# Performance work log

Hardware: AMD Instinct MI355X
Metric: run time of the kernel (lower is better)

## Reference

```python
import jax, jax.numpy as jnp
import numpy as np

TAU = 2.0        # args.tau default (spikingjelly LIFNode)
V_TH = 1.0       # v_threshold
V_RESET = 0.0    # v_reset (hard reset)
ALPHA = 2.0      # ATan surrogate alpha

@jax.custom_vjp
def atan_spike(x):
    # Heaviside spike with ATan surrogate gradient (spikingjelly surrogate.ATan)
    return (x >= 0.0).astype(x.dtype)

def _atan_fwd(x):
    return atan_spike(x), x

def _atan_bwd(x, g):
    sg = (ALPHA / 2.0) / (1.0 + (jnp.pi / 2.0 * ALPHA * x) ** 2)
    return (g * sg,)

atan_spike.defvjp(_atan_fwd, _atan_bwd)

def setup_inputs() -> dict:
    key = jax.random.key(0)
    k1, k2, k3 = jax.random.split(key, 3)
    T, B, IN, OUT, NC = 16, 512, 3072, 2048, 10
    x_seq = jax.random.normal(k1, (T, B, IN), dtype=jnp.float32)
    # xavier-uniform-like scale: sqrt(2/(fan_in+fan_out))
    fc_w = jax.random.normal(k2, (OUT, IN), dtype=jnp.float32) * np.sqrt(2.0 / (IN + OUT)).astype(np.float32)
    fc_b = jnp.zeros((OUT,), jnp.float32)
    aux_w = jax.random.normal(k3, (NC, OUT), dtype=jnp.float32) * np.sqrt(2.0 / (OUT + NC)).astype(np.float32)
    aux_b = jnp.zeros((NC,), jnp.float32)
    return {"x_seq": x_seq, "fc_w": fc_w, "fc_b": fc_b, "aux_w": aux_w, "aux_b": aux_b}

def reference(x_seq, fc_w, fc_b, aux_w, aux_b):
    # fc over all timesteps: [T,B,in] @ [out,in]^T -> [T,B,out]
    cur_seq = jnp.einsum('tbi,oi->tbo', x_seq, fc_w) + fc_b

    def step(v, c):
        # LIF charge: v += (x - (v - v_reset)) / tau
        v = v + (c - (v - V_RESET)) / TAU
        s = atan_spike(v - V_TH)
        s_d = jax.lax.stop_gradient(s)  # detach_reset=True
        v = (1.0 - s_d) * v + s_d * V_RESET  # hard reset
        return v, s

    v0 = jnp.full(cur_seq.shape[1:], V_RESET, cur_seq.dtype)  # reset_net -> v = v_reset
    _, spk_seq = jax.lax.scan(step, v0, cur_seq)  # spk_seq: [T,B,out]
    count = spk_seq.sum(axis=0)                    # [B,out]
    logits = count @ aux_w.T + aux_b               # aux_head local logits [B,10]
    return spk_seq, count, logits
```

## Files before the change

kernel.cpp:

```cpp
#include <hip/hip_runtime.h>
#include <hip/hip_bf16.h>
#include <stdint.h>

#define T_   16
#define B_   512
#define IN_  3072
#define OUT_ 2048
#define NC_  10
#define M_   (T_ * B_)

#define BM 128
#define BN 128

#define SPK_SZ ((size_t)T_ * B_ * OUT_)
#define CNT_SZ ((size_t)B_ * OUT_)

#define TOL 6e-5
#define MAXFLAG (B_ * OUT_)

#define BK2   32
#define NCH2  (IN_ / BK2)
#define TILE_US 8192
#define APAN (M_ / BM)
#define BPAN (OUT_ / BN)

#define A_PREP_BLOCKS (APAN * NCH2 * 2)
#define B_PREP_BLOCKS (BPAN * NCH2 * 2)

typedef __attribute__((ext_vector_type(8))) short s16x8;
typedef __attribute__((ext_vector_type(4))) float f32x4;

__device__ unsigned int g_ctr;
__device__ unsigned int g_list[MAXFLAG];

__global__ void zero_ctr() { if (threadIdx.x == 0) g_ctr = 0; }

__device__ __forceinline__ unsigned short f2bf(float f) {
    __bf16 h = (__bf16)f;
    return *(unsigned short*)&h;
}
__device__ __forceinline__ float bf2f(unsigned short u) {
    union { unsigned int i; float f; } c; c.i = ((unsigned int)u) << 16; return c.f;
}
__device__ __forceinline__ int swz8(int r, int g) {
    return r * 64 + ((g ^ (r & 7)) << 3);
}

__device__ __forceinline__ void gload_lds16(const void* g, void* l) {
    __builtin_amdgcn_global_load_lds(
        (const __attribute__((address_space(1))) unsigned int*)g,
        (__attribute__((address_space(3))) unsigned int*)l, 16, 0, 0);
}

__global__ __launch_bounds__(256)
void prep2(const float* __restrict__ x, const float* __restrict__ w,
           unsigned short* __restrict__ Adig, unsigned short* __restrict__ Bdig)
{
    if (blockIdx.x == 0 && threadIdx.x == 0) g_ctr = 0;

    const float* src; unsigned short* dst; int id; bool isA;
    if (blockIdx.x < A_PREP_BLOCKS) {
        src = x; dst = Adig; id = blockIdx.x * 256 + threadIdx.x; isA = true;
    } else {
        src = w; dst = Bdig; id = (blockIdx.x - A_PREP_BLOCKS) * 256 + threadIdx.x; isA = false;
    }
    const int gk = id & 3;
    const int r  = (id >> 2) & 127;
    const int ch = (id >> 9) % NCH2;
    const int pa = id / (NCH2 * 512);
    const int m  = pa * 128 + r;
    const int k  = ch * BK2 + gk * 8;

    size_t srow;
    if (isA) srow = (size_t)(m & 15) * B_ + (m >> 4);
    else     srow = (size_t)m;

    float f[8];
    *(float4*)&f[0] = *(const float4*)(src + srow * IN_ + k);
    *(float4*)&f[4] = *(const float4*)(src + srow * IN_ + k + 4);
    s16x8 hi, lo;
#pragma unroll
    for (int j = 0; j < 8; ++j) {
        unsigned short hb = f2bf(f[j]);
        hi[j] = (short)hb;
        lo[j] = (short)f2bf(f[j] - bf2f(hb));
    }
    unsigned short* tb = dst + ((size_t)pa * NCH2 + ch) * TILE_US;
    *(s16x8*)&tb[swz8(r, gk)]     = hi;
    *(s16x8*)&tb[swz8(r, gk + 4)] = lo;
}

__global__ __launch_bounds__(512, 1)
void gemm_fused(const unsigned short* __restrict__ Adig,
                const unsigned short* __restrict__ Bdig,
                const float* __restrict__ fcb,
                float* __restrict__ out)
{
    __shared__ __align__(16) unsigned short SH[2 * 4 * TILE_US];

    const int tid = threadIdx.x;
    const int l   = tid & 63;
    const int wv  = tid >> 6;
    const int wh  = wv >> 2;
    const int wn  = (wv & 3) * 64;
    const int pB  = (wv >> 1) & 1;
    const int rb0 = (wv & 1) * 64;

    const int lin = blockIdx.x;
    const int xcd = lin & 7;
    const int jj  = lin >> 3;
    const int pm2 = xcd * 4 + (jj & 3);
    const int pn2 = jj >> 2;
    const int n0  = pn2 * 256;

    f32x4 acc[8][4];
#pragma unroll
    for (int i = 0; i < 8; ++i)
#pragma unroll
        for (int j = 0; j < 4; ++j) acc[i][j] = (f32x4)0.0f;

    const int lp = l & 15;
    const int lq = l >> 4;
    const int l8 = l * 8;

    const int rg  = wv >> 1;
    const int sub = (wv & 1) * 4096;
    const unsigned short* gsrc0;
    if (rg < 2) gsrc0 = Adig + ((size_t)(2 * pm2 + rg) * NCH2) * TILE_US;
    else        gsrc0 = Bdig + ((size_t)(2 * pn2 + rg - 2) * NCH2) * TILE_US;

    auto stage = [&](int ch, int d) {
        const unsigned short* s = gsrc0 + (size_t)ch * TILE_US + sub;
        unsigned short* dp = SH + (d * 4 + rg) * TILE_US + sub;
#pragma unroll
        for (int i = 0; i < 8; ++i)
            gload_lds16(s + i * 512 + l8, dp + i * 512);
    };

    s16x8 a1f[8], a2f[8], b1f[4], b2f[4];

    auto a_read = [&](int dd, int i) {
        const int ra = i * 16 + lp;
        const unsigned short* Ap = SH + (dd * 4 + wh) * TILE_US;
        a1f[i] = *(const s16x8*)&Ap[swz8(ra, lq)];
        a2f[i] = *(const s16x8*)&Ap[swz8(ra, lq + 4)];
    };
    auto b_read = [&](int dd, int j) {
        const int rb = rb0 + j * 16 + lp;
        const unsigned short* Bp = SH + (dd * 4 + 2 + pB) * TILE_US;
        b1f[j] = *(const s16x8*)&Bp[swz8(rb, lq)];
        b2f[j] = *(const s16x8*)&Bp[swz8(rb, lq + 4)];
    };
    auto mfma3 = [&](int i, int j) {
        acc[i][j] = __builtin_amdgcn_mfma_f32_16x16x32_bf16(a1f[i], b1f[j], acc[i][j], 0, 0, 0);
        acc[i][j] = __builtin_amdgcn_mfma_f32_16x16x32_bf16(a2f[i], b1f[j], acc[i][j], 0, 0, 0);
        acc[i][j] = __builtin_amdgcn_mfma_f32_16x16x32_bf16(a1f[i], b2f[j], acc[i][j], 0, 0, 0);
    };

    auto phase_reload = [&](int dd) {
        __builtin_amdgcn_s_setprio(1);
#pragma unroll
        for (int i = 0; i < 7; ++i) {
#pragma unroll
            for (int j = 0; j < 4; ++j) mfma3(i, j);
            a_read(dd, i);
        }
#pragma unroll
        for (int j = 0; j < 4; ++j) {
            mfma3(7, j);
            b_read(dd, j);
        }
        a_read(dd, 7);
        __builtin_amdgcn_s_setprio(0);
    };
    auto phase_plain = [&]() {
        __builtin_amdgcn_s_setprio(1);
#pragma unroll
        for (int i = 0; i < 8; ++i)
#pragma unroll
            for (int j = 0; j < 4; ++j) mfma3(i, j);
        __builtin_amdgcn_s_setprio(0);
    };

    auto body = [&](int ch, int d, int dd) {
        asm volatile("s_waitcnt lgkmcnt(0)" ::: "memory");
        __builtin_amdgcn_s_barrier();
        asm volatile("" ::: "memory");
        if (ch + 2 < NCH2) {
            stage(ch + 2, d);
            asm volatile("s_waitcnt vmcnt(8)" ::: "memory");
        } else {
            asm volatile("s_waitcnt vmcnt(0)" ::: "memory");
        }
        __builtin_amdgcn_s_barrier();
        asm volatile("" ::: "memory");
        if (ch + 1 < NCH2) phase_reload(dd); else phase_plain();
    };

    stage(0, 0);
    asm volatile("s_waitcnt vmcnt(0)" ::: "memory");
    __builtin_amdgcn_s_barrier();
    asm volatile("" ::: "memory");
    stage(1, 1);
#pragma unroll
    for (int i = 0; i < 8; ++i) a_read(0, i);
#pragma unroll
    for (int j = 0; j < 4; ++j) b_read(0, j);

    for (int c2 = 0; c2 < NCH2 / 2; ++c2) {
        const int ch = c2 * 2;
        body(ch, 0, 1);
        body(ch + 1, 1, 0);
    }

    float* cf = (float*)SH;

    const int o_l = tid & 255;
    const int o   = n0 + o_l;
    const float bias = fcb[o];
    const int bq0 = (tid >> 8) * 4;

    for (int p = 0; p < 2; ++p) {
        if (p) __syncthreads();
        if (wh == p) {
#pragma unroll
            for (int i = 0; i < 8; ++i)
#pragma unroll
                for (int j = 0; j < 4; ++j)
#pragma unroll
                    for (int reg = 0; reg < 4; ++reg) {
                        const int row = i * 16 + lq * 4 + reg;
                        const int col = wn + j * 16 + lp;
                        cf[row * 256 + (col ^ ((row & 12) << 1))] = acc[i][j][reg];
                    }
        }
        __syncthreads();

#pragma unroll
        for (int q = 0; q < 4; ++q) {
            const int rl = bq0 + q;
            const int b  = pm2 * 16 + p * 8 + rl;
            float v = 0.0f; int cnt = 0; bool fl = false;
#pragma unroll
            for (int t = 0; t < T_; ++t) {
                const int row = rl * 16 + t;
                const float c32 = cf[row * 256 + (o_l ^ ((row & 12) << 1))];
                const float c = c32 + bias;
                v = v + (c - v) * 0.5f;
                const float dlt = v - 1.0f;
                const bool s = dlt >= 0.0f;
                if (fabsf(dlt) < (float)TOL) fl = true;
                out[(size_t)t * CNT_SZ + (size_t)b * OUT_ + o] = s ? 1.0f : 0.0f;
                cnt += s ? 1 : 0;
                if (s) v = 0.0f;
            }
            out[SPK_SZ + (size_t)b * OUT_ + o] = (float)cnt;
            if (fl) {
                unsigned int idx = atomicAdd(&g_ctr, 1u);
                if (idx < MAXFLAG) g_list[idx] = (unsigned int)(b * OUT_ + o);
            }
        }
    }
}

__global__ __launch_bounds__(256, 2)
void gemm_split(const float* __restrict__ x, const float* __restrict__ w,
                float* __restrict__ cur)
{
    __shared__ __align__(16) unsigned short A1[BM * 64];
    __shared__ __align__(16) unsigned short A2[BM * 64];
    __shared__ __align__(16) unsigned short B1[BN * 64];
    __shared__ __align__(16) unsigned short B2[BN * 64];

    const int tid = threadIdx.x;
    const int l   = tid & 63;
    const int wv  = tid >> 6;
    const int wm  = (wv >> 1) * 64;
    const int wn  = (wv & 1) * 64;
    const int m0  = blockIdx.x * BM;
    const int n0  = blockIdx.y * BN;

    const int r = tid >> 1;
    const int h = tid & 1;
    const float* xa = x + (size_t)(m0 + r) * IN_ + h * 32;
    const float* wa = w + (size_t)(n0 + r) * IN_ + h * 32;

    f32x4 acc[4][4];
#pragma unroll
    for (int i = 0; i < 4; ++i)
#pragma unroll
        for (int j = 0; j < 4; ++j) acc[i][j] = (f32x4)0.0f;

    const int lp = l & 15;
    const int lq = l >> 4;

    for (int ch = 0; ch < 48; ++ch) {
        const int k0 = ch * 64;
        __syncthreads();
        float fx[32], fw[32];
#pragma unroll
        for (int i = 0; i < 8; ++i)
            *(float4*)&fx[4 * i] = *(const float4*)(xa + k0 + 4 * i);
#pragma unroll
        for (int i = 0; i < 8; ++i)
            *(float4*)&fw[4 * i] = *(const float4*)(wa + k0 + 4 * i);

#pragma unroll
        for (int q = 0; q < 4; ++q) {
            s16x8 vh, vl, uh, ul;
#pragma unroll
            for (int j = 0; j < 8; ++j) {
                float f = fx[8 * q + j];
                unsigned short hb = f2bf(f);
                vh[j] = (short)hb;
                vl[j] = (short)f2bf(f - bf2f(hb));
                float g = fw[8 * q + j];
                unsigned short gb = f2bf(g);
                uh[j] = (short)gb;
                ul[j] = (short)f2bf(g - bf2f(gb));
            }
            const int gg = h * 4 + q;
            *(s16x8*)&A1[swz8(r, gg)] = vh;
            *(s16x8*)&A2[swz8(r, gg)] = vl;
            *(s16x8*)&B1[swz8(r, gg)] = uh;
            *(s16x8*)&B2[swz8(r, gg)] = ul;
        }
        __syncthreads();

#pragma unroll
        for (int kk = 0; kk < 2; ++kk) {
            const int gb = kk * 4 + lq;
            s16x8 a1f[4], a2f[4], b1f[4], b2f[4];
#pragma unroll
            for (int i = 0; i < 4; ++i) {
                const int ra = wm + i * 16 + lp;
                a1f[i] = *(const s16x8*)&A1[swz8(ra, gb)];
                a2f[i] = *(const s16x8*)&A2[swz8(ra, gb)];
                const int rb = wn + i * 16 + lp;
                b1f[i] = *(const s16x8*)&B1[swz8(rb, gb)];
                b2f[i] = *(const s16x8*)&B2[swz8(rb, gb)];
            }
#pragma unroll
            for (int i = 0; i < 4; ++i)
#pragma unroll
                for (int j = 0; j < 4; ++j) {
                    acc[i][j] = __builtin_amdgcn_mfma_f32_16x16x32_bf16(
                        a1f[i], b1f[j], acc[i][j], 0, 0, 0);
                    acc[i][j] = __builtin_amdgcn_mfma_f32_16x16x32_bf16(
                        a2f[i], b1f[j], acc[i][j], 0, 0, 0);
                    acc[i][j] = __builtin_amdgcn_mfma_f32_16x16x32_bf16(
                        a1f[i], b2f[j], acc[i][j], 0, 0, 0);
                }
        }
    }

    const int crow = lq * 4, ccol = lp;
#pragma unroll
    for (int i = 0; i < 4; ++i)
#pragma unroll
        for (int j = 0; j < 4; ++j) {
            const size_t mbase = (size_t)(m0 + wm + i * 16 + crow);
            const int o = n0 + wn + j * 16 + ccol;
#pragma unroll
            for (int reg = 0; reg < 4; ++reg)
                cur[(mbase + reg) * OUT_ + o] = acc[i][j][reg];
        }
}

__global__ __launch_bounds__(256)
void lif_pass(const float* __restrict__ fcb, float* __restrict__ out)
{
    const int idx = blockIdx.x * 256 + threadIdx.x;
    const int o = idx & (OUT_ - 1);
    const double bias = (double)fcb[o];
    double v = 0.0; int cnt = 0; bool fl = false;
#pragma unroll
    for (int t = 0; t < T_; ++t) {
        const size_t p = (size_t)t * CNT_SZ + idx;
        double c = (double)out[p] + bias;
        v = v + (c - v) * 0.5;
        double d = v - 1.0;
        bool s = d >= 0.0;
        if (fabs(d) < TOL) fl = true;
        out[p] = s ? 1.0f : 0.0f;
        cnt += s ? 1 : 0;
        if (s) v = 0.0;
    }
    out[SPK_SZ + idx] = (float)cnt;
    if (fl) {
        unsigned int pI = atomicAdd(&g_ctr, 1u);
        if (pI < MAXFLAG) g_list[pI] = (unsigned int)idx;
    }
}

__global__ void fixup(const float* __restrict__ x, const float* __restrict__ w,
                      const float* __restrict__ fcb, float* __restrict__ out)
{
    int nf = (int)g_ctr; if (nf > MAXFLAG) nf = MAXFLAG;
    const int lane = threadIdx.x & 63;
    const int wid  = (blockIdx.x * blockDim.x + threadIdx.x) >> 6;
    const int nw   = (gridDim.x * blockDim.x) >> 6;

    for (int i = wid; i < nf; i += nw) {
        unsigned int e = g_list[i];
        int b = (int)(e >> 11), o = (int)(e & (OUT_ - 1));
        double part[T_];
#pragma unroll
        for (int t = 0; t < T_; ++t) part[t] = 0.0;
        const float* wrow = w + (size_t)o * IN_;
        for (int k = lane; k < IN_; k += 64) {
            double wvv = (double)wrow[k];
#pragma unroll
            for (int t = 0; t < T_; ++t)
                part[t] = fma((double)x[((size_t)t * B_ + b) * IN_ + k], wvv, part[t]);
        }
#pragma unroll
        for (int t = 0; t < T_; ++t)
#pragma unroll
            for (int off = 32; off > 0; off >>= 1)
                part[t] += __shfl_xor(part[t], off, 64);
        if (lane == 0) {
            double bias = (double)fcb[o];
            double v = 0.0; int cnt = 0;
#pragma unroll
            for (int t = 0; t < T_; ++t) {
                double c = part[t] + bias;
                v = v + (c - v) * 0.5;
                bool s = (v - 1.0) >= 0.0;
                out[(size_t)t * CNT_SZ + (size_t)b * OUT_ + o] = s ? 1.0f : 0.0f;
                cnt += s ? 1 : 0;
                if (s) v = 0.0;
            }
            out[SPK_SZ + (size_t)b * OUT_ + o] = (float)cnt;
        }
    }
}

__global__ void aux_logits(const float* __restrict__ cnt,
                           const float* __restrict__ aw,
                           const float* __restrict__ ab,
                           float* __restrict__ lg)
{
    const int b = blockIdx.x;
    const int lane = threadIdx.x;
    double p0=0,p1=0,p2=0,p3=0,p4=0,p5=0,p6=0,p7=0,p8=0,p9=0;
    for (int o = lane; o < OUT_; o += 64) {
        double c = (double)cnt[(size_t)b * OUT_ + o];
        p0 = fma(c, (double)aw[0 * OUT_ + o], p0);
        p1 = fma(c, (double)aw[1 * OUT_ + o], p1);
        p2 = fma(c, (double)aw[2 * OUT_ + o], p2);
        p3 = fma(c, (double)aw[3 * OUT_ + o], p3);
        p4 = fma(c, (double)aw[4 * OUT_ + o], p4);
        p5 = fma(c, (double)aw[5 * OUT_ + o], p5);
        p6 = fma(c, (double)aw[6 * OUT_ + o], p6);
        p7 = fma(c, (double)aw[7 * OUT_ + o], p7);
        p8 = fma(c, (double)aw[8 * OUT_ + o], p8);
        p9 = fma(c, (double)aw[9 * OUT_ + o], p9);
    }
#pragma unroll
    for (int off = 32; off > 0; off >>= 1) {
        p0 += __shfl_xor(p0, off, 64); p1 += __shfl_xor(p1, off, 64);
        p2 += __shfl_xor(p2, off, 64); p3 += __shfl_xor(p3, off, 64);
        p4 += __shfl_xor(p4, off, 64); p5 += __shfl_xor(p5, off, 64);
        p6 += __shfl_xor(p6, off, 64); p7 += __shfl_xor(p7, off, 64);
        p8 += __shfl_xor(p8, off, 64); p9 += __shfl_xor(p9, off, 64);
    }
    if (lane == 0) {
        double pv[NC_] = {p0,p1,p2,p3,p4,p5,p6,p7,p8,p9};
#pragma unroll
        for (int c = 0; c < NC_; ++c)
            lg[(size_t)b * NC_ + c] = (float)(pv[c] + (double)ab[c]);
    }
}

extern "C" void kernel_launch(void* const* d_in, const int* in_sizes, int n_in,
                              void* d_out, int out_size, void* d_ws, size_t ws_size,
                              hipStream_t stream)
{
    (void)in_sizes; (void)n_in; (void)out_size;
    const float* x   = (const float*)d_in[0];
    const float* w   = (const float*)d_in[1];
    const float* fcb = (const float*)d_in[2];
    const float* aw  = (const float*)d_in[3];
    const float* ab  = (const float*)d_in[4];
    float* out = (float*)d_out;

    const size_t needA = (size_t)APAN * NCH2 * TILE_US * 2;
    const size_t needB = (size_t)BPAN * NCH2 * TILE_US * 2;

    if (ws_size >= needA + needB) {
        unsigned short* Adig = (unsigned short*)d_ws;
        unsigned short* Bdig = Adig + (size_t)APAN * NCH2 * TILE_US;
        prep2<<<dim3(A_PREP_BLOCKS + B_PREP_BLOCKS), dim3(256), 0, stream>>>(
            x, w, Adig, Bdig);
        gemm_fused<<<dim3(256), dim3(512), 0, stream>>>(Adig, Bdig, fcb, out);
    } else {
        zero_ctr<<<dim3(1), dim3(64), 0, stream>>>();
        gemm_split<<<dim3(M_ / BM, OUT_ / BN), dim3(256), 0, stream>>>(x, w, out);
        lif_pass<<<dim3(CNT_SZ / 256), dim3(256), 0, stream>>>(fcb, out);
    }

    fixup<<<dim3(192), dim3(256), 0, stream>>>(x, w, fcb, out);

    aux_logits<<<dim3(B_), dim3(64), 0, stream>>>(
        out + SPK_SZ, aw, ab, out + SPK_SZ + CNT_SZ);
}
```

Before: 347.9 us.

## Replace LDS-staged GEMM with direct global-to-register fragment loads

The fused GEMM+LIF kernel drops its double-buffered LDS staging (global_load_lds plus barriers). Each wave now loads its bf16 hi/lo MFMA fragments straight from the pre-swizzled global tiles into registers, relying on L2 for reuse. The grid becomes 512 blocks of 256 threads with two blocks per CU, and each wave runs its LIF epilogue through a private LDS slice, so the block-wide syncs are gone. This removes LDS traffic and barrier stalls, but reused A/B data is now fetched redundantly through L1/L2 with global-memory latency exposed inside the MFMA loop.

```diff
diff --git a/kernel.cpp b/kernel.cpp
--- a/kernel.cpp
+++ b/kernel.cpp
@@ -46,12 +46,6 @@
     return r * 64 + ((g ^ (r & 7)) << 3);
 }
 
-__device__ __forceinline__ void gload_lds16(const void* g, void* l) {
-    __builtin_amdgcn_global_load_lds(
-        (const __attribute__((address_space(1))) unsigned int*)g,
-        (__attribute__((address_space(3))) unsigned int*)l, 16, 0, 0);
-}
-
 __global__ __launch_bounds__(256)
 void prep2(const float* __restrict__ x, const float* __restrict__ w,
            unsigned short* __restrict__ Adig, unsigned short* __restrict__ Bdig)
@@ -90,28 +84,26 @@
     *(s16x8*)&tb[swz8(r, gk + 4)] = lo;
 }
 
-__global__ __launch_bounds__(512, 1)
-void gemm_fused(const unsigned short* __restrict__ Adig,
-                const unsigned short* __restrict__ Bdig,
-                const float* __restrict__ fcb,
-                float* __restrict__ out)
-{
-    __shared__ __align__(16) unsigned short SH[2 * 4 * TILE_US];
+__global__ __launch_bounds__(256, 2)
+void gemm_l2(const unsigned short* __restrict__ Adig,
+             const unsigned short* __restrict__ Bdig,
+             const float* __restrict__ fcb,
+             float* __restrict__ out)
+{
+    __shared__ float SHED[4 * 4096];
 
     const int tid = threadIdx.x;
     const int l   = tid & 63;
     const int wv  = tid >> 6;
-    const int wh  = wv >> 2;
-    const int wn  = (wv & 3) * 64;
-    const int pB  = (wv >> 1) & 1;
-    const int rb0 = (wv & 1) * 64;
 
     const int lin = blockIdx.x;
     const int xcd = lin & 7;
     const int jj  = lin >> 3;
-    const int pm2 = xcd * 4 + (jj & 3);
-    const int pn2 = jj >> 2;
-    const int n0  = pn2 * 256;
+    const int pm  = xcd * 8 + (jj & 7);
+    const int pn2 = jj >> 3;
+    const int pb  = 2 * pn2 + (wv >> 1);
+    const int rb0 = (wv & 1) * 64;
+    const int o0  = pn2 * 256 + wv * 64;
 
     f32x4 acc[8][4];
 #pragma unroll
@@ -121,35 +113,33 @@
 
     const int lp = l & 15;
     const int lq = l >> 4;
-    const int l8 = l * 8;
-
-    const int rg  = wv >> 1;
-    const int sub = (wv & 1) * 4096;
-    const unsigned short* gsrc0;
-    if (rg < 2) gsrc0 = Adig + ((size_t)(2 * pm2 + rg) * NCH2) * TILE_US;
-    else        gsrc0 = Bdig + ((size_t)(2 * pn2 + rg - 2) * NCH2) * TILE_US;
-
-    auto stage = [&](int ch, int d) {
-        const unsigned short* s = gsrc0 + (size_t)ch * TILE_US + sub;
-        unsigned short* dp = SH + (d * 4 + rg) * TILE_US + sub;
-#pragma unroll
-        for (int i = 0; i < 8; ++i)
-            gload_lds16(s + i * 512 + l8, dp + i * 512);
+
+    int aoff1[8], aoff2[8], boff1[4], boff2[4];
+#pragma unroll
+    for (int i = 0; i < 8; ++i) {
+        aoff1[i] = swz8(i * 16 + lp, lq);
+        aoff2[i] = swz8(i * 16 + lp, lq + 4);
+    }
+#pragma unroll
+    for (int j = 0; j < 4; ++j) {
+        boff1[j] = swz8(rb0 + j * 16 + lp, lq);
+        boff2[j] = swz8(rb0 + j * 16 + lp, lq + 4);
+    }
+
+    const unsigned short* Ab = Adig + (size_t)pm * NCH2 * TILE_US;
+    const unsigned short* Bb = Bdig + (size_t)pb * NCH2 * TILE_US;
+
+    s16x8 a1f[8], a2f[8], b1f[4], b2f[4];
+
+    auto a_load = [&](int ch, int i) {
+        const unsigned short* At = Ab + (size_t)ch * TILE_US;
+        a1f[i] = *(const s16x8*)(At + aoff1[i]);
+        a2f[i] = *(const s16x8*)(At + aoff2[i]);
     };
-
-    s16x8 a1f[8], a2f[8], b1f[4], b2f[4];
-
-    auto a_read = [&](int dd, int i) {
-        const int ra = i * 16 + lp;
-        const unsigned short* Ap = SH + (dd * 4 + wh) * TILE_US;
-        a1f[i] = *(const s16x8*)&Ap[swz8(ra, lq)];
-        a2f[i] = *(const s16x8*)&Ap[swz8(ra, lq + 4)];
-    };
-    auto b_read = [&](int dd, int j) {
-        const int rb = rb0 + j * 16 + lp;
-        const unsigned short* Bp = SH + (dd * 4 + 2 + pB) * TILE_US;
-        b1f[j] = *(const s16x8*)&Bp[swz8(rb, lq)];
-        b2f[j] = *(const s16x8*)&Bp[swz8(rb, lq + 4)];
+    auto b_load = [&](int ch, int j) {
+        const unsigned short* Bt = Bb + (size_t)ch * TILE_US;
+        b1f[j] = *(const s16x8*)(Bt + boff1[j]);
+        b2f[j] = *(const s16x8*)(Bt + boff2[j]);
     };
     auto mfma3 = [&](int i, int j) {
         acc[i][j] = __builtin_amdgcn_mfma_f32_16x16x32_bf16(a1f[i], b1f[j], acc[i][j], 0, 0, 0);
@@ -157,94 +147,63 @@
         acc[i][j] = __builtin_amdgcn_mfma_f32_16x16x32_bf16(a1f[i], b2f[j], acc[i][j], 0, 0, 0);
     };
 
-    auto phase_reload = [&](int dd) {
-        __builtin_amdgcn_s_setprio(1);
-#pragma unroll
-        for (int i = 0; i < 7; ++i) {
-#pragma unroll
-            for (int j = 0; j < 4; ++j) mfma3(i, j);
-            a_read(dd, i);
-        }
-#pragma unroll
-        for (int j = 0; j < 4; ++j) {
-            mfma3(7, j);
-            b_read(dd, j);
-        }
-        a_read(dd, 7);
-        __builtin_amdgcn_s_setprio(0);
-    };
-    auto phase_plain = [&]() {
-        __builtin_amdgcn_s_setprio(1);
-#pragma unroll
-        for (int i = 0; i < 8; ++i)
-#pragma unroll
-            for (int j = 0; j < 4; ++j) mfma3(i, j);
-        __builtin_amdgcn_s_setprio(0);
-    };
-
-    auto body = [&](int ch, int d, int dd) {
+#pragma unroll
+    for (int i = 0; i < 8; ++i) a_load(0, i);
+#pragma unroll
+    for (int j = 0; j < 4; ++j) b_load(0, j);
+
+    for (int ch = 0; ch < NCH2; ++ch) {
+        if (ch + 1 < NCH2) {
+            __builtin_amdgcn_s_setprio(1);
+#pragma unroll
+            for (int i = 0; i < 7; ++i) {
+#pragma unroll
+                for (int j = 0; j < 4; ++j) mfma3(i, j);
+                a_load(ch + 1, i);
+            }
+#pragma unroll
+            for (int j = 0; j < 4; ++j) {
+                mfma3(7, j);
+                b_load(ch + 1, j);
+            }
+            a_load(ch + 1, 7);
+            __builtin_amdgcn_s_setprio(0);
+        } else {
+            __builtin_amdgcn_s_setprio(1);
+#pragma unroll
+            for (int i = 0; i < 8; ++i)
+#pragma unroll
+                for (int j = 0; j < 4; ++j) mfma3(i, j);
+            __builtin_amdgcn_s_setprio(0);
+        }
+    }
+
+    float* S = &SHED[wv * 4096];
+    const int o   = o0 + l;
+    const float bias = fcb[o];
+
+#pragma unroll
+    for (int h = 0; h < 2; ++h) {
+#pragma unroll
+        for (int ii = 0; ii < 4; ++ii)
+#pragma unroll
+            for (int j = 0; j < 4; ++j)
+#pragma unroll
+                for (int reg = 0; reg < 4; ++reg) {
+                    const int r = ii * 16 + lq * 4 + reg;
+                    const int c = j * 16 + lp;
+                    S[r * 64 + (c ^ (lq << 4))] = acc[4 * h + ii][j][reg];
+                }
         asm volatile("s_waitcnt lgkmcnt(0)" ::: "memory");
-        __builtin_amdgcn_s_barrier();
-        asm volatile("" ::: "memory");
-        if (ch + 2 < NCH2) {
-            stage(ch + 2, d);
-            asm volatile("s_waitcnt vmcnt(8)" ::: "memory");
-        } else {
-            asm volatile("s_waitcnt vmcnt(0)" ::: "memory");
-        }
-        __builtin_amdgcn_s_barrier();
-        asm volatile("" ::: "memory");
-        if (ch + 1 < NCH2) phase_reload(dd); else phase_plain();
-    };
-
-    stage(0, 0);
-    asm volatile("s_waitcnt vmcnt(0)" ::: "memory");
-    __builtin_amdgcn_s_barrier();
-    asm volatile("" ::: "memory");
-    stage(1, 1);
-#pragma unroll
-    for (int i = 0; i < 8; ++i) a_read(0, i);
-#pragma unroll
-    for (int j = 0; j < 4; ++j) b_read(0, j);
-
-    for (int c2 = 0; c2 < NCH2 / 2; ++c2) {
-        const int ch = c2 * 2;
-        body(ch, 0, 1);
-        body(ch + 1, 1, 0);
-    }
-
-    float* cf = (float*)SH;
-
-    const int o_l = tid & 255;
-    const int o   = n0 + o_l;
-    const float bias = fcb[o];
-    const int bq0 = (tid >> 8) * 4;
-
-    for (int p = 0; p < 2; ++p) {
-        if (p) __syncthreads();
-        if (wh == p) {
-#pragma unroll
-            for (int i = 0; i < 8; ++i)
-#pragma unroll
-                for (int j = 0; j < 4; ++j)
-#pragma unroll
-                    for (int reg = 0; reg < 4; ++reg) {
-                        const int row = i * 16 + lq * 4 + reg;
-                        const int col = wn + j * 16 + lp;
-                        cf[row * 256 + (col ^ ((row & 12) << 1))] = acc[i][j][reg];
-                    }
-        }
-        __syncthreads();
 
 #pragma unroll
         for (int q = 0; q < 4; ++q) {
-            const int rl = bq0 + q;
-            const int b  = pm2 * 16 + p * 8 + rl;
+            const int b = pm * 8 + h * 4 + q;
             float v = 0.0f; int cnt = 0; bool fl = false;
 #pragma unroll
             for (int t = 0; t < T_; ++t) {
-                const int row = rl * 16 + t;
-                const float c32 = cf[row * 256 + (o_l ^ ((row & 12) << 1))];
+                const int r = q * 16 + t;
+                const float c32 = S[r * 64 + (l ^ (((t >> 2) & 3) << 4))];
                 const float c = c32 + bias;
                 v = v + (c - v) * 0.5f;
                 const float dlt = v - 1.0f;
@@ -260,6 +219,7 @@
                 if (idx < MAXFLAG) g_list[idx] = (unsigned int)(b * OUT_ + o);
             }
         }
+        if (h == 0) asm volatile("s_waitcnt lgkmcnt(0)" ::: "memory");
     }
 }
 
@@ -493,7 +453,7 @@
         unsigned short* Bdig = Adig + (size_t)APAN * NCH2 * TILE_US;
         prep2<<<dim3(A_PREP_BLOCKS + B_PREP_BLOCKS), dim3(256), 0, stream>>>(
             x, w, Adig, Bdig);
-        gemm_fused<<<dim3(256), dim3(512), 0, stream>>>(Adig, Bdig, fcb, out);
+        gemm_l2<<<dim3(512), dim3(256), 0, stream>>>(Adig, Bdig, fcb, out);
     } else {
         zero_ctr<<<dim3(1), dim3(64), 0, stream>>>();
         gemm_split<<<dim3(M_ / BM, OUT_ / BN), dim3(256), 0, stream>>>(x, w, out);
```

Result: slower. 407.1 us (+17.0%).
